# Kernel optimization log

Measured on AMD Instinct MI355X. Metric: run time of the kernel, lower is better.

## Reference

```python
import jax, jax.numpy as jnp
import numpy as np

N = 2048        # samples per batch
IN = 256        # in_size
OUT = 256       # out_size
T = 128         # num_tasks


def setup_inputs() -> dict:
    key = jax.random.key(0)
    k1, k2, k3 = jax.random.split(key, 3)
    inputs = jax.random.normal(k1, (N, IN), dtype=jnp.float32)
    task_ids = jax.random.randint(k2, (N,), 0, T, dtype=jnp.int64)
    # Task-specific weight table [num_tasks, in_size, out_size],
    # kaiming-style scale 1/sqrt(in_size).
    W = jax.random.normal(k3, (T, IN, OUT), dtype=jnp.float32) / jnp.sqrt(
        jnp.float32(IN)
    )
    return {"inputs": inputs, "task_ids": task_ids, "W": W}


def reference(inputs, task_ids, W):
    # _get_matrices: gather per-sample weight matrix by task id -> [N, in, out]
    mats = W[task_ids]
    # einsum 'ni,nio->no': per-sample matvec
    return jnp.einsum("ni,nio->no", inputs, mats)
```

## Files before the change

kernel.cpp:

```cpp
#include <hip/hip_runtime.h>
#include <hip/hip_bf16.h>


#define NSAMP 2048
#define NTASK 128
#define INSZ  256
#define OUTSZ 256
#define CHUNK 8
#define MAXC  6

__global__ __launch_bounds__(256, 3)
void TaskSpecificLinear_24910810316924_kernel(
    const float* __restrict__ X,
    const int*   __restrict__ ids32,
    const float* __restrict__ W,
    float*       __restrict__ out)
{
    __shared__ int   s_ids[NSAMP];
    __shared__ float xt[INSZ * CHUNK];
    __shared__ float pacc[4 * CHUNK * 128];
    __shared__ int   scanbuf[256];
    __shared__ int   s_list[CHUNK];
    __shared__ int   s_odd;

    const int tid  = threadIdx.x;
    const int t    = blockIdx.x;
    const int c    = blockIdx.y;
    const int half = blockIdx.z;

    if (tid == 0) s_odd = 0;
    __syncthreads();

    {
        int any = 0;
        for (int j = 1 + 2 * tid; j < NSAMP; j += 512) any |= ids32[j];
        if (any) s_odd = 1;
    }
    __syncthreads();
    const bool is64 = (s_odd == 0);

    if (is64) {
        #pragma unroll
        for (int j = 0; j < 8; ++j) {
            int n = tid + 256 * j;
            s_ids[n] = ((const int2*)ids32)[n].x;
        }
    } else {
        #pragma unroll
        for (int j = 0; j < 8; ++j) {
            int n = tid + 256 * j;
            s_ids[n] = ids32[n];
        }
    }
    __syncthreads();

    int match[8];
    int localcnt = 0;
    #pragma unroll
    for (int j = 0; j < 8; ++j) {
        match[j] = (s_ids[tid * 8 + j] == t);
        localcnt += match[j];
    }
    scanbuf[tid] = localcnt;
    __syncthreads();
    #pragma unroll
    for (int off = 1; off < 256; off <<= 1) {
        int v = scanbuf[tid];
        if (tid >= off) v += scanbuf[tid - off];
        __syncthreads();
        scanbuf[tid] = v;
        __syncthreads();
    }
    const int count = scanbuf[255];
    const int len   = min(CHUNK, count - c * CHUNK);
    if (len <= 0) return;

    if (tid < CHUNK) s_list[tid] = -1;
    __syncthreads();
    {
        int rank = scanbuf[tid] - localcnt;
        #pragma unroll
        for (int j = 0; j < 8; ++j) {
            if (match[j]) {
                int r = rank++;
                if (r >= c * CHUNK && r < c * CHUNK + CHUNK)
                    s_list[r - c * CHUNK] = tid * 8 + j;
            }
        }
    }
    __syncthreads();

    #pragma unroll
    for (int s = 0; s < CHUNK; ++s) {
        int n = s_list[s];
        float v = 0.f;
        if (n >= 0) v = X[(size_t)n * INSZ + tid];
        xt[tid * CHUNK + s] = v;
    }
    __syncthreads();

    const int lane = tid & 63;
    const int wv   = tid >> 6;
    const int col0 = half * 128 + lane * 2;
    const float* wp = W + ((size_t)t * INSZ + wv * 64) * OUTSZ + col0;

    float2 acc[CHUNK];
    #pragma unroll
    for (int s = 0; s < CHUNK; ++s) acc[s] = make_float2(0.f, 0.f);

    #pragma unroll 8
    for (int i = 0; i < 64; ++i) {
        const float2 w2 = *(const float2*)wp;
        const float4 xa = *(const float4*)&xt[(wv * 64 + i) * CHUNK];
        const float4 xb = *(const float4*)&xt[(wv * 64 + i) * CHUNK + 4];
        acc[0].x += xa.x * w2.x; acc[0].y += xa.x * w2.y;
        acc[1].x += xa.y * w2.x; acc[1].y += xa.y * w2.y;
        acc[2].x += xa.z * w2.x; acc[2].y += xa.z * w2.y;
        acc[3].x += xa.w * w2.x; acc[3].y += xa.w * w2.y;
        acc[4].x += xb.x * w2.x; acc[4].y += xb.x * w2.y;
        acc[5].x += xb.y * w2.x; acc[5].y += xb.y * w2.y;
        acc[6].x += xb.z * w2.x; acc[6].y += xb.z * w2.y;
        acc[7].x += xb.w * w2.x; acc[7].y += xb.w * w2.y;
        wp += OUTSZ;
    }

    float* pb = &pacc[wv * (CHUNK * 128) + lane * 2];
    #pragma unroll
    for (int s = 0; s < CHUNK; ++s)
        *(float2*)&pb[s * 128] = acc[s];
    __syncthreads();

    {
        const int e = tid * 4;
        float4 v = make_float4(0.f, 0.f, 0.f, 0.f);
        #pragma unroll
        for (int w2i = 0; w2i < 4; ++w2i) {
            const float4 p = *(const float4*)&pacc[w2i * 1024 + e];
            v.x += p.x; v.y += p.y; v.z += p.z; v.w += p.w;
        }
        const int s  = e >> 7;
        const int lc = e & 127;
        const int n  = s_list[s];
        if (n >= 0)
            *(float4*)&out[(size_t)n * OUTSZ + half * 128 + lc] = v;
    }
}

extern "C" void kernel_launch(void* const* d_in, const int* in_sizes, int n_in,
                              void* d_out, int out_size, void* d_ws, size_t ws_size,
                              hipStream_t stream) {
    const float* X   = (const float*)d_in[0];
    const int*   ids = (const int*)d_in[1];
    const float* W   = (const float*)d_in[2];
    float*       out = (float*)d_out;

    dim3 grid(NTASK, MAXC, 2);
    dim3 block(256, 1, 1);
    TaskSpecificLinear_24910810316924_kernel<<<grid, block, 0, stream>>>(X, ids, W, out);
}
```

Measured before the change: 87.57 us.

## Replace LDS prefix scan with wave ballots and merge output halves into one block

The shared-memory Hillock-style scan (16 barriers) and the staged id buffer are replaced by per-wave ballot/popcount ranking, with one barrier to exchange wave totals. Id matching now reads global ids directly, and the 64-bit-detection probe is shrunk to one load per thread. The grid's half dimension is removed so each block computes both 128-column halves in a loop. This halves the redundant id scanning and X staging per block, at the cost of half as many blocks and longer serial work per block. The probe sampling fewer odd words risks misdetecting the int32/int64 format in rare cases.

```diff
diff --git a/kernel.cpp b/kernel.cpp
--- a/kernel.cpp
+++ b/kernel.cpp
@@ -16,76 +16,66 @@
     const float* __restrict__ W,
     float*       __restrict__ out)
 {
-    __shared__ int   s_ids[NSAMP];
     __shared__ float xt[INSZ * CHUNK];
     __shared__ float pacc[4 * CHUNK * 128];
-    __shared__ int   scanbuf[256];
     __shared__ int   s_list[CHUNK];
+    __shared__ int   s_wcnt[4];
     __shared__ int   s_odd;
 
     const int tid  = threadIdx.x;
     const int t    = blockIdx.x;
     const int c    = blockIdx.y;
-    const int half = blockIdx.z;
+    const int lane = tid & 63;
+    const int wv   = tid >> 6;
 
     if (tid == 0) s_odd = 0;
+    if (tid < CHUNK) s_list[tid] = -1;
     __syncthreads();
 
-    {
-        int any = 0;
-        for (int j = 1 + 2 * tid; j < NSAMP; j += 512) any |= ids32[j];
-        if (any) s_odd = 1;
-    }
+    if (ids32[1 + 8 * tid]) s_odd = 1;
     __syncthreads();
     const bool is64 = (s_odd == 0);
 
-    if (is64) {
-        #pragma unroll
-        for (int j = 0; j < 8; ++j) {
-            int n = tid + 256 * j;
-            s_ids[n] = ((const int2*)ids32)[n].x;
-        }
-    } else {
-        #pragma unroll
-        for (int j = 0; j < 8; ++j) {
-            int n = tid + 256 * j;
-            s_ids[n] = ids32[n];
+    int match[8];
+    {
+        if (is64) {
+            #pragma unroll
+            for (int j = 0; j < 8; ++j)
+                match[j] = (((const int2*)ids32)[tid * 8 + j].x == t);
+        } else {
+            #pragma unroll
+            for (int j = 0; j < 8; ++j)
+                match[j] = (ids32[tid * 8 + j] == t);
         }
     }
+
+    unsigned long long mask[8];
+    int wave_total = 0;
+    #pragma unroll
+    for (int j = 0; j < 8; ++j) {
+        mask[j] = __ballot(match[j]);
+        wave_total += __popcll(mask[j]);
+    }
+    if (lane == 0) s_wcnt[wv] = wave_total;
     __syncthreads();
 
-    int match[8];
-    int localcnt = 0;
-    #pragma unroll
-    for (int j = 0; j < 8; ++j) {
-        match[j] = (s_ids[tid * 8 + j] == t);
-        localcnt += match[j];
-    }
-    scanbuf[tid] = localcnt;
-    __syncthreads();
-    #pragma unroll
-    for (int off = 1; off < 256; off <<= 1) {
-        int v = scanbuf[tid];
-        if (tid >= off) v += scanbuf[tid - off];
-        __syncthreads();
-        scanbuf[tid] = v;
-        __syncthreads();
-    }
-    const int count = scanbuf[255];
+    const int b0 = s_wcnt[0], b1 = s_wcnt[1], b2 = s_wcnt[2], b3 = s_wcnt[3];
+    const int count = b0 + b1 + b2 + b3;
     const int len   = min(CHUNK, count - c * CHUNK);
     if (len <= 0) return;
 
-    if (tid < CHUNK) s_list[tid] = -1;
-    __syncthreads();
     {
-        int rank = scanbuf[tid] - localcnt;
+        int r = (wv > 0 ? b0 : 0) + (wv > 1 ? b1 : 0) + (wv > 2 ? b2 : 0);
+        const unsigned long long below = (1ULL << lane) - 1ULL;
         #pragma unroll
         for (int j = 0; j < 8; ++j) {
             if (match[j]) {
-                int r = rank++;
-                if (r >= c * CHUNK && r < c * CHUNK + CHUNK)
-                    s_list[r - c * CHUNK] = tid * 8 + j;
+                int rank = r + __popcll(mask[j] & below);
+                int rr = rank - c * CHUNK;
+                if (rr >= 0 && rr < CHUNK)
+                    s_list[rr] = tid * 8 + j;
             }
+            r += __popcll(mask[j]);
         }
     }
     __syncthreads();
@@ -99,50 +89,51 @@
     }
     __syncthreads();
 
-    const int lane = tid & 63;
-    const int wv   = tid >> 6;
-    const int col0 = half * 128 + lane * 2;
-    const float* wp = W + ((size_t)t * INSZ + wv * 64) * OUTSZ + col0;
+    for (int half = 0; half < 2; ++half) {
+        const int col0 = half * 128 + lane * 2;
+        const float* wp = W + ((size_t)t * INSZ + wv * 64) * OUTSZ + col0;
 
-    float2 acc[CHUNK];
-    #pragma unroll
-    for (int s = 0; s < CHUNK; ++s) acc[s] = make_float2(0.f, 0.f);
+        float2 acc[CHUNK];
+        #pragma unroll
+        for (int s = 0; s < CHUNK; ++s) acc[s] = make_float2(0.f, 0.f);
 
-    #pragma unroll 8
-    for (int i = 0; i < 64; ++i) {
-        const float2 w2 = *(const float2*)wp;
-        const float4 xa = *(const float4*)&xt[(wv * 64 + i) * CHUNK];
-        const float4 xb = *(const float4*)&xt[(wv * 64 + i) * CHUNK + 4];
-        acc[0].x += xa.x * w2.x; acc[0].y += xa.x * w2.y;
-        acc[1].x += xa.y * w2.x; acc[1].y += xa.y * w2.y;
-        acc[2].x += xa.z * w2.x; acc[2].y += xa.z * w2.y;
-        acc[3].x += xa.w * w2.x; acc[3].y += xa.w * w2.y;
-        acc[4].x += xb.x * w2.x; acc[4].y += xb.x * w2.y;
-        acc[5].x += xb.y * w2.x; acc[5].y += xb.y * w2.y;
-        acc[6].x += xb.z * w2.x; acc[6].y += xb.z * w2.y;
-        acc[7].x += xb.w * w2.x; acc[7].y += xb.w * w2.y;
-        wp += OUTSZ;
-    }
+        #pragma unroll 8
+        for (int i = 0; i < 64; ++i) {
+            const float2 w2 = *(const float2*)wp;
+            const float4 xa = *(const float4*)&xt[(wv * 64 + i) * CHUNK];
+            const float4 xb = *(const float4*)&xt[(wv * 64 + i) * CHUNK + 4];
+            acc[0].x += xa.x * w2.x; acc[0].y += xa.x * w2.y;
+            acc[1].x += xa.y * w2.x; acc[1].y += xa.y * w2.y;
+            acc[2].x += xa.z * w2.x; acc[2].y += xa.z * w2.y;
+            acc[3].x += xa.w * w2.x; acc[3].y += xa.w * w2.y;
+            acc[4].x += xb.x * w2.x; acc[4].y += xb.x * w2.y;
+            acc[5].x += xb.y * w2.x; acc[5].y += xb.y * w2.y;
+            acc[6].x += xb.z * w2.x; acc[6].y += xb.z * w2.y;
+            acc[7].x += xb.w * w2.x; acc[7].y += xb.w * w2.y;
+            wp += OUTSZ;
+        }
 
-    float* pb = &pacc[wv * (CHUNK * 128) + lane * 2];
-    #pragma unroll
-    for (int s = 0; s < CHUNK; ++s)
-        *(float2*)&pb[s * 128] = acc[s];
-    __syncthreads();
+        float* pb = &pacc[wv * (CHUNK * 128) + lane * 2];
+        #pragma unroll
+        for (int s = 0; s < CHUNK; ++s)
+            *(float2*)&pb[s * 128] = acc[s];
+        __syncthreads();
 
-    {
-        const int e = tid * 4;
-        float4 v = make_float4(0.f, 0.f, 0.f, 0.f);
-        #pragma unroll
-        for (int w2i = 0; w2i < 4; ++w2i) {
-            const float4 p = *(const float4*)&pacc[w2i * 1024 + e];
-            v.x += p.x; v.y += p.y; v.z += p.z; v.w += p.w;
+        {
+            const int e = tid * 4;
+            float4 v = make_float4(0.f, 0.f, 0.f, 0.f);
+            #pragma unroll
+            for (int w2i = 0; w2i < 4; ++w2i) {
+                const float4 p = *(const float4*)&pacc[w2i * 1024 + e];
+                v.x += p.x; v.y += p.y; v.z += p.z; v.w += p.w;
+            }
+            const int s  = e >> 7;
+            const int lc = e & 127;
+            const int n  = s_list[s];
+            if (n >= 0)
+                *(float4*)&out[(size_t)n * OUTSZ + half * 128 + lc] = v;
         }
-        const int s  = e >> 7;
-        const int lc = e & 127;
-        const int n  = s_list[s];
-        if (n >= 0)
-            *(float4*)&out[(size_t)n * OUTSZ + half * 128 + lc] = v;
+        __syncthreads();
     }
 }
 
@@ -154,7 +145,7 @@
     const float* W   = (const float*)d_in[2];
     float*       out = (float*)d_out;
 
-    dim3 grid(NTASK, MAXC, 2);
+    dim3 grid(NTASK, MAXC, 1);
     dim3 block(256, 1, 1);
     TaskSpecificLinear_24910810316924_kernel<<<grid, block, 0, stream>>>(X, ids, W, out);
 }
```

Result: faster. 85.69 us (-2.1%).
